# Kernel tuning notes

Hardware: AMD Instinct MI355X
Metric: run time of the kernel (lower is better)

Reference implementation:

```python
import jax, jax.numpy as jnp
import numpy as np

E, H, F, N, B = 512, 8, 2048, 1024, 4
HD = E // H


def setup_inputs() -> dict:
    key = jax.random.key(0)
    ks = jax.random.split(key, 20)
    s = 0.02
    return {
        "node_inputs": jax.random.normal(ks[0], (N, B, E), jnp.float32),
        "parent_mask": jax.random.uniform(ks[1], (B, N, N), jnp.float32),
        "hidden": jax.random.bernoulli(ks[2], 0.5, (B, N, N)),
        "pad_mask": jax.random.bernoulli(ks[3], 0.1, (B, N)),
        "Wp": jax.random.normal(ks[4], (H, E), jnp.float32) * s,
        "bp": jnp.zeros((H,), jnp.float32),
        "Wc": jax.random.normal(ks[5], (H, E), jnp.float32) * s,
        "bc": jnp.zeros((H,), jnp.float32),
        "Wqkv": jax.random.normal(ks[6], (3 * E, E), jnp.float32) * s,
        "bqkv": jnp.zeros((3 * E,), jnp.float32),
        "Wo": jax.random.normal(ks[7], (E, E), jnp.float32) * s,
        "bo": jnp.zeros((E,), jnp.float32),
        "W1": jax.random.normal(ks[8], (F, E), jnp.float32) * s,
        "b1": jnp.zeros((F,), jnp.float32),
        "W2": jax.random.normal(ks[9], (E, F), jnp.float32) * s,
        "b2": jnp.zeros((E,), jnp.float32),
        "ln1_g": jnp.ones((E,), jnp.float32),
        "ln1_b": jnp.zeros((E,), jnp.float32),
        "ln2_g": jnp.ones((E,), jnp.float32),
        "ln2_b": jnp.zeros((E,), jnp.float32),
    }


def _layer_norm(x, g, b, eps=1e-5):
    m = jnp.mean(x, axis=-1, keepdims=True)
    v = jnp.mean((x - m) ** 2, axis=-1, keepdims=True)
    return (x - m) * jax.lax.rsqrt(v + eps) * g + b


def reference(node_inputs, parent_mask, hidden, pad_mask, Wp, bp, Wc, bc,
              Wqkv, bqkv, Wo, bo, W1, b1, W2, b2, ln1_g, ln1_b, ln2_g, ln2_b):
    x = node_inputs  # (N, B, E), seq-first like nn.TransformerEncoderLayer
    # parent/child per-head biases: Linear(E->H), permuted to (B, H, N)
    pbias = jnp.transpose(x @ Wp.T + bp, (1, 2, 0))
    cbias = jnp.transpose(x @ Wc.T + bc, (1, 2, 0))
    # additive attention bias (B, H, N, N)
    am = (jnp.swapaxes(parent_mask, 1, 2)[:, None] * pbias[..., None]
          + parent_mask[:, None] * cbias[..., None])
    am = jnp.where(hidden[:, None], -jnp.inf, am)
    # multi-head self-attention
    qkv = x @ Wqkv.T + bqkv  # (N, B, 3E)
    q, k, v = jnp.split(qkv, 3, axis=-1)

    def heads(t):  # (N, B, E) -> (B, H, N, HD)
        return jnp.transpose(t.reshape(N, B, H, HD), (1, 2, 0, 3))

    q, k, v = heads(q), heads(k), heads(v)
    scores = jnp.einsum("bhqd,bhkd->bhqk", q, k) / jnp.sqrt(jnp.float32(HD)) + am
    scores = jnp.where(pad_mask[:, None, None, :], -jnp.inf, scores)
    attn = jax.nn.softmax(scores, axis=-1)
    ctx = jnp.einsum("bhqk,bhkd->bhqd", attn, v)  # (B, H, N, HD)
    ctx = jnp.transpose(ctx, (2, 0, 1, 3)).reshape(N, B, E)
    attn_out = ctx @ Wo.T + bo
    # post-norm transformer encoder layer (dropout=0, relu activation)
    y = _layer_norm(x + attn_out, ln1_g, ln1_b)
    ff = jax.nn.relu(y @ W1.T + b1) @ W2.T + b2
    return _layer_norm(y + ff, ln2_g, ln2_b)
```

## Files before the change

### kernel.cpp

```cpp
#include <hip/hip_runtime.h>
#include <hip/hip_bf16.h>
#include <stdint.h>

using bf16 = __hip_bfloat16;

typedef __bf16 bf16x8 __attribute__((ext_vector_type(8)));
typedef float  f32x4  __attribute__((ext_vector_type(4)));

__device__ __forceinline__ float bflo(uint32_t u) { return __uint_as_float(u << 16); }
__device__ __forceinline__ float bfhi(uint32_t u) { return __uint_as_float(u & 0xffff0000u); }

__device__ __forceinline__ void load8(const bf16* p, float* f) {
  uint4 u = *(const uint4*)p;
  f[0] = bflo(u.x); f[1] = bfhi(u.x);
  f[2] = bflo(u.y); f[3] = bfhi(u.y);
  f[4] = bflo(u.z); f[5] = bfhi(u.z);
  f[6] = bflo(u.w); f[7] = bfhi(u.w);
}
__device__ __forceinline__ void load8(const float* p, float* f) {
  float4 a = *(const float4*)p, b = *(const float4*)(p + 4);
  f[0] = a.x; f[1] = a.y; f[2] = a.z; f[3] = a.w;
  f[4] = b.x; f[5] = b.y; f[6] = b.z; f[7] = b.w;
}
__device__ __forceinline__ void store1(float* o, float v) { *o = v; }
__device__ __forceinline__ void store1(bf16* o, float v) { *o = __float2bfloat16(v); }
__device__ __forceinline__ uint32_t bfbits(float x) {
  bf16 v = __float2bfloat16(x);
  return (uint32_t)*(uint16_t*)&v;
}

typedef const uint32_t __attribute__((address_space(1)))* gp_t;
typedef uint32_t __attribute__((address_space(3)))* lp_t;
__device__ __forceinline__ void gload16(const void* g, void* l) {
  __builtin_amdgcn_global_load_lds((gp_t)g, (lp_t)l, 16, 0, 0);
}

__global__ __launch_bounds__(256)
void cvt5(const float* __restrict__ s0, const float* __restrict__ s1,
          const float* __restrict__ s2, const float* __restrict__ s3,
          const float* __restrict__ s4, bf16* __restrict__ d0,
          bf16* __restrict__ d1, bf16* __restrict__ d2,
          bf16* __restrict__ d3, bf16* __restrict__ d4)
{
  size_t j = ((size_t)blockIdx.x * 256 + threadIdx.x) * 8;
  const float* s; bf16* o; size_t off;
  if      (j < 2097152) { s = s0; o = d0; off = j; }
  else if (j < 2883584) { s = s1; o = d1; off = j - 2097152; }
  else if (j < 3145728) { s = s2; o = d2; off = j - 2883584; }
  else if (j < 4194304) { s = s3; o = d3; off = j - 3145728; }
  else                  { s = s4; o = d4; off = j - 4194304; }
  float f[8];
  load8(s + off, f);
  uint4 u;
  u.x = (bfbits(f[1]) << 16) | bfbits(f[0]);
  u.y = (bfbits(f[3]) << 16) | bfbits(f[2]);
  u.z = (bfbits(f[5]) << 16) | bfbits(f[4]);
  u.w = (bfbits(f[7]) << 16) | bfbits(f[6]);
  *(uint4*)(o + off) = u;
}

__global__ __launch_bounds__(256)
void prep_small(const float* __restrict__ Wp, const float* __restrict__ Wc,
                const float* __restrict__ bqkv, const float* __restrict__ bp,
                const float* __restrict__ bc, bf16* __restrict__ wq,
                float* __restrict__ bias_ext)
{
  if (blockIdx.x < 2) {
    int j = (blockIdx.x * 256 + threadIdx.x) * 8;
    if (j < 4096) {
      float f[8]; load8(Wp + j, f);
#pragma unroll
      for (int i = 0; i < 8; ++i) wq[(size_t)1536 * 512 + j + i] = __float2bfloat16(f[i]);
    }
  } else if (blockIdx.x < 4) {
    int j = ((blockIdx.x - 2) * 256 + threadIdx.x) * 8;
    if (j < 4096) {
      float f[8]; load8(Wc + j, f);
#pragma unroll
      for (int i = 0; i < 8; ++i) wq[(size_t)1544 * 512 + j + i] = __float2bfloat16(f[i]);
    }
  } else {
    int j = threadIdx.x * 8;
#pragma unroll
    for (int i = 0; i < 8; ++i) {
      int cc = j + i;
      if (cc < 1664) {
        float v = 0.f;
        if (cc < 1536) v = bqkv[cc];
        else if (cc < 1544) v = bp[cc - 1536];
        else if (cc < 1552) v = bc[cc - 1544];
        bias_ext[cc] = v;
      }
    }
  }
}

__global__ __launch_bounds__(256)
void mask_pack(const float* __restrict__ pm, const int* __restrict__ hid,
               const int* __restrict__ padm, uint32_t* __restrict__ out)
{
  __shared__ float tileT[128][65];
  const int b = blockIdx.z, q0 = blockIdx.y * 64, k0 = blockIdx.x * 128;
  const int t = threadIdx.x;
  const size_t pb = (size_t)b << 20;
#pragma unroll
  for (int i = 0; i < 32; ++i) {
    int idx = t + i * 256;
    int r = idx >> 6, c = idx & 63;
    tileT[r][c] = pm[pb + (size_t)(k0 + r) * 1024 + q0 + c];
  }
  __syncthreads();
#pragma unroll
  for (int i = 0; i < 32; ++i) {
    int idx = t + i * 256;
    int q = idx >> 7, k = idx & 127;
    size_t src = pb + (size_t)(q0 + q) * 1024 + k0 + k;
    int msk = hid[src] | padm[b * 1024 + k0 + k];
    uint32_t u = 0xFFFFFFFFu;
    if (!msk) u = (bfbits(tileT[k][q]) << 16) | bfbits(pm[src]);
    out[src] = u;
  }
}

template<int MODE, int BN>
__global__ __launch_bounds__(256)
void gemm_bt(const bf16* __restrict__ A, const bf16* __restrict__ W,
             const float* __restrict__ bias, bf16* __restrict__ outb,
             float* __restrict__ outf, int M, int Nout, int K, int kLen)
{
  constexpr int NT = BN / 32;
  __shared__ bf16 As[128 * 64];
  __shared__ bf16 Bs[BN * 64];
  const int t = threadIdx.x, lane = t & 63, wave = t >> 6;
  const int m0 = blockIdx.y * 128, n0 = blockIdx.x * BN;
  const int kOff = blockIdx.z * kLen;
  if (MODE == 3) outf += (size_t)blockIdx.z * M * Nout;
  const int wr = wave >> 1, wc = wave & 1;
  const int frow = lane & 15, ksel = (lane >> 4) * 8;
  f32x4 acc[4 * NT] = {};
  const bf16* Ab = A + (size_t)m0 * K;
  const bf16* Wb = W + (size_t)n0 * K;

  for (int k0 = kOff; k0 < kOff + kLen; k0 += 64) {
    __syncthreads();
#pragma unroll
    for (int i = 0; i < 4; ++i) {
      int ib = i * 256 + wave * 64;
      int idx = ib + lane;
      gload16(Ab + (size_t)(idx >> 3) * K + k0 + (idx & 7) * 8, As + ib * 8);
    }
#pragma unroll
    for (int i = 0; i < BN / 32; ++i) {
      int ib = i * 256 + wave * 64;
      int idx = ib + lane;
      gload16(Wb + (size_t)(idx >> 3) * K + k0 + (idx & 7) * 8, Bs + ib * 8);
    }
    __syncthreads();
#pragma unroll
    for (int kk = 0; kk < 64; kk += 32) {
      bf16x8 af[4], bf_[NT];
#pragma unroll
      for (int mt = 0; mt < 4; ++mt)
        af[mt] = *(const bf16x8*)(As + (wr * 64 + mt * 16 + frow) * 64 + kk + ksel);
#pragma unroll
      for (int nt = 0; nt < NT; ++nt)
        bf_[nt] = *(const bf16x8*)(Bs + (wc * (BN / 2) + nt * 16 + frow) * 64 + kk + ksel);
#pragma unroll
      for (int mt = 0; mt < 4; ++mt)
#pragma unroll
        for (int nt = 0; nt < NT; ++nt)
          acc[mt * NT + nt] = __builtin_amdgcn_mfma_f32_16x16x32_bf16(
              af[mt], bf_[nt], acc[mt * NT + nt], 0, 0, 0);
    }
  }
  const int rb = (lane >> 4) * 4, cb = lane & 15;
#pragma unroll
  for (int mt = 0; mt < 4; ++mt)
#pragma unroll
    for (int nt = 0; nt < NT; ++nt) {
      f32x4 a = acc[mt * NT + nt];
#pragma unroll
      for (int r = 0; r < 4; ++r) {
        int row = m0 + wr * 64 + mt * 16 + rb + r;
        int col = n0 + wc * (BN / 2) + nt * 16 + cb;
        if (MODE == 3) {
          outf[(size_t)row * Nout + col] = a[r];
        } else {
          float v = a[r] + bias[col];
          if (MODE == 1) v = fmaxf(v, 0.f);
          if (MODE == 2) {
            if (col >= 1552) continue;
            int n = row >> 2, b = row & 3;
            if (col >= 1536) {
              int j = col - 1536;
              int hh = j & 7;
              outf[(j < 8 ? 0 : 32768) + (b * 8 + hh) * 1024 + n] = v;
            } else {
              int which = col >> 9, hh = (col >> 6) & 7, d = col & 63;
              if (which == 0) v *= 0.125f;
              size_t idx;
              if (which == 2)
                idx = (((size_t)(64 + b * 8 + hh)) << 16) + (size_t)d * 1024 + n;
              else
                idx = (((size_t)(which * 32 + b * 8 + hh)) << 16) + (size_t)n * 64 + d;
              outb[idx] = __float2bfloat16(v);
            }
          } else {
            outb[(size_t)row * Nout + col] = __float2bfloat16(v);
          }
        }
      }
    }
}

__global__ __launch_bounds__(256, 3)
void attn_mfma(const bf16* __restrict__ qkv, const float* __restrict__ pbw,
               const float* __restrict__ cbw, const uint32_t* __restrict__ mpk,
               bf16* __restrict__ ctxo)
{
  __shared__ bf16 Kt[128 * 64];
  __shared__ bf16 Vt[64 * 128];
  __shared__ bf16 Ps[4][16][136];
  const int t = threadIdx.x, lane = t & 63, wave = t >> 6;
  const int g = lane >> 4, c = lane & 15;
  const int h = blockIdx.y, b = blockIdx.z;
  const int q0 = blockIdx.x * 64 + wave * 16;
  const size_t bh = (size_t)b * 8 + h;
  const bf16* Qp = qkv + (bh << 16);
  const bf16* Kp = qkv + ((32 + bh) << 16);
  const bf16* Vg = qkv + ((64 + bh) << 16);

  bf16x8 qa0 = *(const bf16x8*)(Qp + (size_t)(q0 + c) * 64 + g * 8);
  bf16x8 qa1 = *(const bf16x8*)(Qp + (size_t)(q0 + c) * 64 + 32 + g * 8);

  const float pbq = pbw[bh * 1024 + q0 + c];
  const float cbq = cbw[bh * 1024 + q0 + c];
  const uint32_t* mrp = mpk + (((size_t)b * 1024 + q0 + c) << 10);

  f32x4 oacc[4] = {{0,0,0,0},{0,0,0,0},{0,0,0,0},{0,0,0,0}};
  float m = -1e30f, l = 0.f;

  for (int kt = 0; kt < 8; ++kt) {
    const int k0 = kt * 128;
    __syncthreads();
#pragma unroll
    for (int i = 0; i < 4; ++i) {
      int ib = i * 256 + wave * 64;
      int idx = ib + lane;
      int r = idx >> 3, p = idx & 7;
      gload16(Kp + (size_t)(k0 + r) * 64 + ((p ^ (r & 7)) * 8), Kt + ib * 8);
    }
#pragma unroll
    for (int i = 0; i < 4; ++i) {
      int ib = i * 256 + wave * 64;
      int idx = ib + lane;
      int d = idx >> 4, p = idx & 15;
      gload16(Vg + (size_t)d * 1024 + k0 + ((p ^ (d & 15)) * 8), Vt + ib * 8);
    }
    uint4 mu[8];
#pragma unroll
    for (int nt = 0; nt < 8; ++nt)
      mu[nt] = *(const uint4*)(mrp + k0 + nt * 16 + 4 * g);
    __syncthreads();
    f32x4 sacc[8];
#pragma unroll
    for (int nt = 0; nt < 8; ++nt) {
      f32x4 z = {0.f,0.f,0.f,0.f};
      int r = nt * 16 + c;
      bf16x8 k0f = *(const bf16x8*)(Kt + r * 64 + (( g      ^ (c & 7)) * 8));
      bf16x8 k1f = *(const bf16x8*)(Kt + r * 64 + (((4 + g) ^ (c & 7)) * 8));
      z = __builtin_amdgcn_mfma_f32_16x16x32_bf16(k0f, qa0, z, 0, 0, 0);
      z = __builtin_amdgcn_mfma_f32_16x16x32_bf16(k1f, qa1, z, 0, 0, 0);
      sacc[nt] = z;
    }
    float mx = -1e30f;
#pragma unroll
    for (int nt = 0; nt < 8; ++nt) {
      uint32_t uu[4] = {mu[nt].x, mu[nt].y, mu[nt].z, mu[nt].w};
#pragma unroll
      for (int r = 0; r < 4; ++r) {
        float s = sacc[nt][r] + bfhi(uu[r]) * pbq + bflo(uu[r]) * cbq;
        s = (uu[r] == 0xFFFFFFFFu) ? -1e30f : s;
        sacc[nt][r] = s;
        mx = fmaxf(mx, s);
      }
    }
    mx = fmaxf(mx, __shfl_xor(mx, 16));
    mx = fmaxf(mx, __shfl_xor(mx, 32));
    const float newm = fmaxf(m, mx);
    const float al = __expf(m - newm);
    float ps = 0.f;
#pragma unroll
    for (int nt = 0; nt < 8; ++nt) {
      float p0 = (sacc[nt][0] <= -1e29f) ? 0.f : __expf(sacc[nt][0] - newm);
      float p1 = (sacc[nt][1] <= -1e29f) ? 0.f : __expf(sacc[nt][1] - newm);
      float p2 = (sacc[nt][2] <= -1e29f) ? 0.f : __expf(sacc[nt][2] - newm);
      float p3 = (sacc[nt][3] <= -1e29f) ? 0.f : __expf(sacc[nt][3] - newm);
      ps += (p0 + p1) + (p2 + p3);
      uint2 w;
      w.x = (bfbits(p1) << 16) | bfbits(p0);
      w.y = (bfbits(p3) << 16) | bfbits(p2);
      *(uint2*)&Ps[wave][c][nt * 16 + 4 * g] = w;
    }
    ps += __shfl_xor(ps, 16);
    ps += __shfl_xor(ps, 32);
    l = l * al + ps;
    m = newm;
#pragma unroll
    for (int dt = 0; dt < 4; ++dt) {
      oacc[dt][0] *= al; oacc[dt][1] *= al;
      oacc[dt][2] *= al; oacc[dt][3] *= al;
    }
#pragma unroll
    for (int dt = 0; dt < 4; ++dt) {
      int row = dt * 16 + c;
#pragma unroll
      for (int kc = 0; kc < 4; ++kc) {
        bf16x8 vf = *(const bf16x8*)(Vt + row * 128 + (((kc * 4 + g) ^ c) * 8));
        bf16x8 pf = *(const bf16x8*)&Ps[wave][c][kc * 32 + g * 8];
        oacc[dt] = __builtin_amdgcn_mfma_f32_16x16x32_bf16(vf, pf, oacc[dt], 0, 0, 0);
      }
    }
  }
  const float inv = (l > 0.f) ? 1.f / l : 0.f;
  const int qg = q0 + c;
#pragma unroll
  for (int dt = 0; dt < 4; ++dt)
#pragma unroll
    for (int rg = 0; rg < 4; ++rg) {
      int d = dt * 16 + 4 * g + rg;
      ctxo[((size_t)qg * 4 + b) * 512 + h * 64 + d] =
          __float2bfloat16(oacc[dt][rg] * inv);
    }
}

template<typename TA, typename TO>
__global__ __launch_bounds__(256)
void ln_res2(const TA* __restrict__ a, const float* __restrict__ p0,
             const float* __restrict__ p1, const float* __restrict__ bias,
             const float* __restrict__ g, const float* __restrict__ be,
             TO* __restrict__ out)
{
  const int wave = threadIdx.x >> 6, lane = threadIdx.x & 63;
  const int m = blockIdx.x * 4 + wave;
  const size_t base = (size_t)m * 512 + lane * 8;
  float va[8], f0[8], f1[8], bb[8];
  load8(a + base, va);
  load8(p0 + base, f0);
  load8(p1 + base, f1);
  load8(bias + lane * 8, bb);
  float v[8], s = 0.f;
#pragma unroll
  for (int j = 0; j < 8; ++j) { v[j] = va[j] + f0[j] + f1[j] + bb[j]; s += v[j]; }
#pragma unroll
  for (int off = 32; off; off >>= 1) s += __shfl_xor(s, off);
  const float mean = s * (1.f / 512.f);
  float q = 0.f;
#pragma unroll
  for (int j = 0; j < 8; ++j) { float d = v[j] - mean; q += d * d; }
#pragma unroll
  for (int off = 32; off; off >>= 1) q += __shfl_xor(q, off);
  const float rs = rsqrtf(q * (1.f / 512.f) + 1e-5f);
  float gv[8], bv[8];
  load8(g + lane * 8, gv);
  load8(be + lane * 8, bv);
#pragma unroll
  for (int j = 0; j < 8; ++j)
    store1(out + base + j, (v[j] - mean) * rs * gv[j] + bv[j]);
}

extern "C" void kernel_launch(void* const* d_in, const int* in_sizes, int n_in,
                              void* d_out, int out_size, void* d_ws, size_t ws_size,
                              hipStream_t stream)
{
  (void)in_sizes; (void)n_in; (void)out_size; (void)ws_size;
  const float* x    = (const float*)d_in[0];
  const float* pm   = (const float*)d_in[1];
  const int*   hid  = (const int*)d_in[2];
  const int*   padm = (const int*)d_in[3];
  const float* Wp   = (const float*)d_in[4];
  const float* bp   = (const float*)d_in[5];
  const float* Wc   = (const float*)d_in[6];
  const float* bc   = (const float*)d_in[7];
  const float* Wqkv = (const float*)d_in[8];
  const float* bqkv = (const float*)d_in[9];
  const float* Wo   = (const float*)d_in[10];
  const float* bo   = (const float*)d_in[11];
  const float* W1   = (const float*)d_in[12];
  const float* b1   = (const float*)d_in[13];
  const float* W2   = (const float*)d_in[14];
  const float* b2   = (const float*)d_in[15];
  const float* g1   = (const float*)d_in[16];
  const float* be1  = (const float*)d_in[17];
  const float* g2   = (const float*)d_in[18];
  const float* be2  = (const float*)d_in[19];

  char* ws = (char*)d_ws;
  bf16*     qkvb  = (bf16*)    (ws);
  float*    pbo   = (float*)   (ws + 12582912);
  float*    cbo   = (float*)   (ws + 12713984);
  uint32_t* mpk   = (uint32_t*)(ws + 12845056);
  bf16*     ctx   = (bf16*)    (ws + 29622272);
  float*    part  = (float*)   (ws);
  bf16*     ff1   = (bf16*)    (ws + 16777216);
  bf16*     y     = (bf16*)    (ws + 33816576);
  bf16*     xb    = (bf16*)    (ws + 38010880);
  bf16*     wqkvb = (bf16*)    (ws + 42205184);
  bf16*     wob   = (bf16*)    (ws + 43909120);
  bf16*     w1b   = (bf16*)    (ws + 44433408);
  bf16*     w2b   = (bf16*)    (ws + 46530560);
  float*    bext  = (float*)   (ws + 48627712);
  float*    part1 = part + (size_t)4096 * 512;

  cvt5<<<2560, 256, 0, stream>>>(x, Wqkv, Wo, W1, W2, xb, wqkvb, wob, w1b, w2b);
  prep_small<<<5, 256, 0, stream>>>(Wp, Wc, bqkv, bp, bc, wqkvb, bext);
  mask_pack<<<dim3(8, 16, 4), 256, 0, stream>>>(pm, hid, padm, mpk);
  gemm_bt<2, 128><<<dim3(13, 32), 256, 0, stream>>>(xb, wqkvb, bext, qkvb, pbo, 4096, 1664, 512, 512);
  attn_mfma<<<dim3(16, 8, 4), 256, 0, stream>>>(qkvb, pbo, cbo, mpk, ctx);
  gemm_bt<3, 64><<<dim3(8, 32, 2), 256, 0, stream>>>(ctx, wob, nullptr, nullptr, part, 4096, 512, 512, 256);
  ln_res2<float, bf16><<<1024, 256, 0, stream>>>(x, part, part1, bo, g1, be1, y);
  gemm_bt<1, 128><<<dim3(16, 32), 256, 0, stream>>>(y, w1b, b1, ff1, nullptr, 4096, 2048, 512, 512);
  gemm_bt<3, 64><<<dim3(8, 32, 2), 256, 0, stream>>>(ff1, w2b, nullptr, nullptr, part, 4096, 512, 2048, 1024);
  ln_res2<bf16, float><<<1024, 256, 0, stream>>>(y, part, part1, b2, g2, be2, (float*)d_out);
}
```

Baseline: 272.0 us.

## Merge prologue kernels and halve attention key tile for higher occupancy

Fuses the three prologue kernels (mask packing, bulk fp32-to-bf16 conversion, small weight/bias prep) into one launch dispatched by block index, removing two kernel launches. The attention kernel's key/value tile shrinks from 128 to 64 keys, cutting LDS use and the score register arrays so the launch bound can rise from 3 to 6 blocks per SM. The trade-off is twice as many key-loop iterations, each with its own barriers and online-softmax rescale. The fused prologue also gives every block the 33KB transpose tile in shared memory, even blocks that never use it.

```diff
diff --git a/kernel.cpp b/kernel.cpp
--- a/kernel.cpp
+++ b/kernel.cpp
@@ -36,89 +36,85 @@
 }
 
 __global__ __launch_bounds__(256)
-void cvt5(const float* __restrict__ s0, const float* __restrict__ s1,
-          const float* __restrict__ s2, const float* __restrict__ s3,
-          const float* __restrict__ s4, bf16* __restrict__ d0,
-          bf16* __restrict__ d1, bf16* __restrict__ d2,
-          bf16* __restrict__ d3, bf16* __restrict__ d4)
-{
-  size_t j = ((size_t)blockIdx.x * 256 + threadIdx.x) * 8;
-  const float* s; bf16* o; size_t off;
-  if      (j < 2097152) { s = s0; o = d0; off = j; }
-  else if (j < 2883584) { s = s1; o = d1; off = j - 2097152; }
-  else if (j < 3145728) { s = s2; o = d2; off = j - 2883584; }
-  else if (j < 4194304) { s = s3; o = d3; off = j - 3145728; }
-  else                  { s = s4; o = d4; off = j - 4194304; }
-  float f[8];
-  load8(s + off, f);
-  uint4 u;
-  u.x = (bfbits(f[1]) << 16) | bfbits(f[0]);
-  u.y = (bfbits(f[3]) << 16) | bfbits(f[2]);
-  u.z = (bfbits(f[5]) << 16) | bfbits(f[4]);
-  u.w = (bfbits(f[7]) << 16) | bfbits(f[6]);
-  *(uint4*)(o + off) = u;
-}
-
-__global__ __launch_bounds__(256)
-void prep_small(const float* __restrict__ Wp, const float* __restrict__ Wc,
-                const float* __restrict__ bqkv, const float* __restrict__ bp,
-                const float* __restrict__ bc, bf16* __restrict__ wq,
-                float* __restrict__ bias_ext)
-{
-  if (blockIdx.x < 2) {
-    int j = (blockIdx.x * 256 + threadIdx.x) * 8;
-    if (j < 4096) {
-      float f[8]; load8(Wp + j, f);
-#pragma unroll
-      for (int i = 0; i < 8; ++i) wq[(size_t)1536 * 512 + j + i] = __float2bfloat16(f[i]);
-    }
-  } else if (blockIdx.x < 4) {
-    int j = ((blockIdx.x - 2) * 256 + threadIdx.x) * 8;
-    if (j < 4096) {
-      float f[8]; load8(Wc + j, f);
-#pragma unroll
-      for (int i = 0; i < 8; ++i) wq[(size_t)1544 * 512 + j + i] = __float2bfloat16(f[i]);
-    }
-  } else {
-    int j = threadIdx.x * 8;
-#pragma unroll
-    for (int i = 0; i < 8; ++i) {
-      int cc = j + i;
-      if (cc < 1664) {
-        float v = 0.f;
-        if (cc < 1536) v = bqkv[cc];
-        else if (cc < 1544) v = bp[cc - 1536];
-        else if (cc < 1552) v = bc[cc - 1544];
-        bias_ext[cc] = v;
-      }
-    }
-  }
-}
-
-__global__ __launch_bounds__(256)
-void mask_pack(const float* __restrict__ pm, const int* __restrict__ hid,
-               const int* __restrict__ padm, uint32_t* __restrict__ out)
+void prologue(const float* __restrict__ pm, const int* __restrict__ hid,
+              const int* __restrict__ padm, uint32_t* __restrict__ mout,
+              const float* __restrict__ x, const float* __restrict__ Wqkv,
+              const float* __restrict__ Wo, const float* __restrict__ W1,
+              const float* __restrict__ W2, bf16* __restrict__ xb,
+              bf16* __restrict__ wq, bf16* __restrict__ wob,
+              bf16* __restrict__ w1b, bf16* __restrict__ w2b,
+              const float* __restrict__ bqkv, const float* __restrict__ bp,
+              const float* __restrict__ bc, const float* __restrict__ Wp,
+              const float* __restrict__ Wc, float* __restrict__ bias_ext)
 {
   __shared__ float tileT[128][65];
-  const int b = blockIdx.z, q0 = blockIdx.y * 64, k0 = blockIdx.x * 128;
-  const int t = threadIdx.x;
-  const size_t pb = (size_t)b << 20;
-#pragma unroll
-  for (int i = 0; i < 32; ++i) {
-    int idx = t + i * 256;
-    int r = idx >> 6, c = idx & 63;
-    tileT[r][c] = pm[pb + (size_t)(k0 + r) * 1024 + q0 + c];
-  }
-  __syncthreads();
-#pragma unroll
-  for (int i = 0; i < 32; ++i) {
-    int idx = t + i * 256;
-    int q = idx >> 7, k = idx & 127;
-    size_t src = pb + (size_t)(q0 + q) * 1024 + k0 + k;
-    int msk = hid[src] | padm[b * 1024 + k0 + k];
-    uint32_t u = 0xFFFFFFFFu;
-    if (!msk) u = (bfbits(tileT[k][q]) << 16) | bfbits(pm[src]);
-    out[src] = u;
+  const int blk = blockIdx.x, t = threadIdx.x;
+  if (blk < 512) {
+    const int k0 = (blk & 7) * 128, q0 = ((blk >> 3) & 15) * 64, b = blk >> 7;
+    const size_t pb = (size_t)b << 20;
+#pragma unroll
+    for (int i = 0; i < 32; ++i) {
+      int idx = t + i * 256;
+      int r = idx >> 6, c = idx & 63;
+      tileT[r][c] = pm[pb + (size_t)(k0 + r) * 1024 + q0 + c];
+    }
+    __syncthreads();
+#pragma unroll
+    for (int i = 0; i < 32; ++i) {
+      int idx = t + i * 256;
+      int q = idx >> 7, k = idx & 127;
+      size_t src = pb + (size_t)(q0 + q) * 1024 + k0 + k;
+      int msk = hid[src] | padm[b * 1024 + k0 + k];
+      uint32_t u = 0xFFFFFFFFu;
+      if (!msk) u = (bfbits(tileT[k][q]) << 16) | bfbits(pm[src]);
+      mout[src] = u;
+    }
+  } else if (blk < 3072) {
+    size_t j = ((size_t)(blk - 512) * 256 + t) * 8;
+    const float* s; bf16* o; size_t off;
+    if      (j < 2097152) { s = x;    o = xb;  off = j; }
+    else if (j < 2883584) { s = Wqkv; o = wq;  off = j - 2097152; }
+    else if (j < 3145728) { s = Wo;   o = wob; off = j - 2883584; }
+    else if (j < 4194304) { s = W1;   o = w1b; off = j - 3145728; }
+    else                  { s = W2;   o = w2b; off = j - 4194304; }
+    float f[8];
+    load8(s + off, f);
+    uint4 u;
+    u.x = (bfbits(f[1]) << 16) | bfbits(f[0]);
+    u.y = (bfbits(f[3]) << 16) | bfbits(f[2]);
+    u.z = (bfbits(f[5]) << 16) | bfbits(f[4]);
+    u.w = (bfbits(f[7]) << 16) | bfbits(f[6]);
+    *(uint4*)(o + off) = u;
+  } else {
+    int sb = blk - 3072;
+    if (sb < 2) {
+      int j = (sb * 256 + t) * 8;
+      if (j < 4096) {
+        float f[8]; load8(Wp + j, f);
+#pragma unroll
+        for (int i = 0; i < 8; ++i) wq[(size_t)1536 * 512 + j + i] = __float2bfloat16(f[i]);
+      }
+    } else if (sb < 4) {
+      int j = ((sb - 2) * 256 + t) * 8;
+      if (j < 4096) {
+        float f[8]; load8(Wc + j, f);
+#pragma unroll
+        for (int i = 0; i < 8; ++i) wq[(size_t)1544 * 512 + j + i] = __float2bfloat16(f[i]);
+      }
+    } else {
+      int j = t * 8;
+#pragma unroll
+      for (int i = 0; i < 8; ++i) {
+        int cc = j + i;
+        if (cc < 1664) {
+          float v = 0.f;
+          if (cc < 1536) v = bqkv[cc];
+          else if (cc < 1544) v = bp[cc - 1536];
+          else if (cc < 1552) v = bc[cc - 1544];
+          bias_ext[cc] = v;
+        }
+      }
+    }
   }
 }
 
@@ -213,14 +209,14 @@
     }
 }
 
-__global__ __launch_bounds__(256, 3)
+__global__ __launch_bounds__(256, 6)
 void attn_mfma(const bf16* __restrict__ qkv, const float* __restrict__ pbw,
                const float* __restrict__ cbw, const uint32_t* __restrict__ mpk,
                bf16* __restrict__ ctxo)
 {
-  __shared__ bf16 Kt[128 * 64];
-  __shared__ bf16 Vt[64 * 128];
-  __shared__ bf16 Ps[4][16][136];
+  __shared__ bf16 Kt[64 * 64];
+  __shared__ bf16 Vt[64 * 64];
+  __shared__ bf16 Ps[4][16][72];
   const int t = threadIdx.x, lane = t & 63, wave = t >> 6;
   const int g = lane >> 4, c = lane & 15;
   const int h = blockIdx.y, b = blockIdx.z;
@@ -240,31 +236,31 @@
   f32x4 oacc[4] = {{0,0,0,0},{0,0,0,0},{0,0,0,0},{0,0,0,0}};
   float m = -1e30f, l = 0.f;
 
-  for (int kt = 0; kt < 8; ++kt) {
-    const int k0 = kt * 128;
+  for (int kt = 0; kt < 16; ++kt) {
+    const int k0 = kt * 64;
     __syncthreads();
 #pragma unroll
-    for (int i = 0; i < 4; ++i) {
+    for (int i = 0; i < 2; ++i) {
       int ib = i * 256 + wave * 64;
       int idx = ib + lane;
       int r = idx >> 3, p = idx & 7;
       gload16(Kp + (size_t)(k0 + r) * 64 + ((p ^ (r & 7)) * 8), Kt + ib * 8);
     }
 #pragma unroll
-    for (int i = 0; i < 4; ++i) {
+    for (int i = 0; i < 2; ++i) {
       int ib = i * 256 + wave * 64;
       int idx = ib + lane;
-      int d = idx >> 4, p = idx & 15;
-      gload16(Vg + (size_t)d * 1024 + k0 + ((p ^ (d & 15)) * 8), Vt + ib * 8);
-    }
-    uint4 mu[8];
-#pragma unroll
-    for (int nt = 0; nt < 8; ++nt)
+      int d = idx >> 3, p = idx & 7;
+      gload16(Vg + (size_t)d * 1024 + k0 + ((p ^ (d & 7)) * 8), Vt + ib * 8);
+    }
+    uint4 mu[4];
+#pragma unroll
+    for (int nt = 0; nt < 4; ++nt)
       mu[nt] = *(const uint4*)(mrp + k0 + nt * 16 + 4 * g);
     __syncthreads();
-    f32x4 sacc[8];
-#pragma unroll
-    for (int nt = 0; nt < 8; ++nt) {
+    f32x4 sacc[4];
+#pragma unroll
+    for (int nt = 0; nt < 4; ++nt) {
       f32x4 z = {0.f,0.f,0.f,0.f};
       int r = nt * 16 + c;
       bf16x8 k0f = *(const bf16x8*)(Kt + r * 64 + (( g      ^ (c & 7)) * 8));
@@ -275,7 +271,7 @@
     }
     float mx = -1e30f;
 #pragma unroll
-    for (int nt = 0; nt < 8; ++nt) {
+    for (int nt = 0; nt < 4; ++nt) {
       uint32_t uu[4] = {mu[nt].x, mu[nt].y, mu[nt].z, mu[nt].w};
 #pragma unroll
       for (int r = 0; r < 4; ++r) {
@@ -291,7 +287,7 @@
     const float al = __expf(m - newm);
     float ps = 0.f;
 #pragma unroll
-    for (int nt = 0; nt < 8; ++nt) {
+    for (int nt = 0; nt < 4; ++nt) {
       float p0 = (sacc[nt][0] <= -1e29f) ? 0.f : __expf(sacc[nt][0] - newm);
       float p1 = (sacc[nt][1] <= -1e29f) ? 0.f : __expf(sacc[nt][1] - newm);
       float p2 = (sacc[nt][2] <= -1e29f) ? 0.f : __expf(sacc[nt][2] - newm);
@@ -315,8 +311,8 @@
     for (int dt = 0; dt < 4; ++dt) {
       int row = dt * 16 + c;
 #pragma unroll
-      for (int kc = 0; kc < 4; ++kc) {
-        bf16x8 vf = *(const bf16x8*)(Vt + row * 128 + (((kc * 4 + g) ^ c) * 8));
+      for (int kc = 0; kc < 2; ++kc) {
+        bf16x8 vf = *(const bf16x8*)(Vt + row * 64 + (((kc * 4 + g) ^ (c & 7)) * 8));
         bf16x8 pf = *(const bf16x8*)&Ps[wave][c][kc * 32 + g * 8];
         oacc[dt] = __builtin_amdgcn_mfma_f32_16x16x32_bf16(vf, pf, oacc[dt], 0, 0, 0);
       }
@@ -412,9 +408,9 @@
   float*    bext  = (float*)   (ws + 48627712);
   float*    part1 = part + (size_t)4096 * 512;
 
-  cvt5<<<2560, 256, 0, stream>>>(x, Wqkv, Wo, W1, W2, xb, wqkvb, wob, w1b, w2b);
-  prep_small<<<5, 256, 0, stream>>>(Wp, Wc, bqkv, bp, bc, wqkvb, bext);
-  mask_pack<<<dim3(8, 16, 4), 256, 0, stream>>>(pm, hid, padm, mpk);
+  prologue<<<3077, 256, 0, stream>>>(pm, hid, padm, mpk, x, Wqkv, Wo, W1, W2,
+                                     xb, wqkvb, wob, w1b, w2b,
+                                     bqkv, bp, bc, Wp, Wc, bext);
   gemm_bt<2, 128><<<dim3(13, 32), 256, 0, stream>>>(xb, wqkvb, bext, qkvb, pbo, 4096, 1664, 512, 512);
   attn_mfma<<<dim3(16, 8, 4), 256, 0, stream>>>(qkvb, pbo, cbo, mpk, ctx);
   gemm_bt<3, 64><<<dim3(8, 32, 2), 256, 0, stream>>>(ctx, wob, nullptr, nullptr, part, 4096, 512, 512, 256);
```

Measured after the change: 297.4 us. +9.3%, slower.
